# Performance work log

Measured on AMD Instinct MI355X. Metric: run time of the kernel, lower is better.

The kernel has to match this reference:

```python
import jax, jax.numpy as jnp
import numpy as np

B, H, W, C = 64, 28, 28, 384
NH, WS = 12, 7
KD = C // NH            # key_dim = head_dim = 32 (attn_ratio=1.0 -> d = KD)
QKV_OUT = 3 * KD * NH   # 1152
HID = 4 * C             # mlp hidden
N = WS * WS             # tokens per window
L = H * W
SCALE = KD ** -0.5
EPS_LN = 1e-5
EPS_BN = 1e-5


def _make_bias_idxs():
    pts = [(i, j) for i in range(WS) for j in range(WS)]
    offs, idxs = {}, []
    for p1 in pts:
        for p2 in pts:
            o = (abs(p1[0] - p2[0]), abs(p1[1] - p2[1]))
            if o not in offs:
                offs[o] = len(offs)
            idxs.append(offs[o])
    return np.asarray(idxs, dtype=np.int32).reshape(N, N)


def _ln(x, g, b):
    m = jnp.mean(x, axis=-1, keepdims=True)
    v = jnp.mean(jnp.square(x - m), axis=-1, keepdims=True)
    return (x - m) * jax.lax.rsqrt(v + EPS_LN) * g + b


def setup_inputs() -> dict:
    key = jax.random.key(0)
    ks = jax.random.split(key, 8)
    s = 0.02
    return {
        "x": jax.random.normal(ks[0], (B, L, C), jnp.float32),
        "ln_a_g": jnp.ones((C,), jnp.float32),
        "ln_a_b": jnp.zeros((C,), jnp.float32),
        "qkv_w": jax.random.normal(ks[1], (QKV_OUT, C), jnp.float32) * s,
        "qkv_b": jnp.zeros((QKV_OUT,), jnp.float32),
        "attn_bias": jax.random.normal(ks[2], (NH, N), jnp.float32) * s,
        "proj_w": jax.random.normal(ks[3], (C, C), jnp.float32) * s,
        "proj_b": jnp.zeros((C,), jnp.float32),
        "conv_w": jax.random.normal(ks[4], (C, 1, 3, 3), jnp.float32) * s,
        "bn_g": jnp.ones((C,), jnp.float32),
        "bn_b": jnp.zeros((C,), jnp.float32),
        "bn_m": jnp.zeros((C,), jnp.float32),
        "bn_v": jnp.ones((C,), jnp.float32),
        "ln_m_g": jnp.ones((C,), jnp.float32),
        "ln_m_b": jnp.zeros((C,), jnp.float32),
        "fc1_w": jax.random.normal(ks[5], (HID, C), jnp.float32) * s,
        "fc1_b": jnp.zeros((HID,), jnp.float32),
        "fc2_w": jax.random.normal(ks[6], (C, HID), jnp.float32) * s,
        "fc2_b": jnp.zeros((C,), jnp.float32),
        "bias_idxs": jnp.asarray(_make_bias_idxs()),
    }


def reference(x, ln_a_g, ln_a_b, qkv_w, qkv_b, attn_bias, proj_w, proj_b,
              conv_w, bn_g, bn_b, bn_m, bn_v, ln_m_g, ln_m_b,
              fc1_w, fc1_b, fc2_w, fc2_b, bias_idxs):
    res = x
    nh, nw = H // WS, W // WS
    # window partition: [B,L,C] -> [B*nWin, N, C]
    xw = x.reshape(B, nh, WS, nw, WS, C).transpose(0, 1, 3, 2, 4, 5)
    xw = xw.reshape(B * nh * nw, N, C)
    # attention
    xn = _ln(xw, ln_a_g, ln_a_b)
    qkv = xn @ qkv_w.T + qkv_b                       # [Bw, N, 3*NH*KD]
    qkv = qkv.reshape(-1, N, NH, 3 * KD).transpose(0, 2, 1, 3)
    q, k, v = qkv[..., :KD], qkv[..., KD:2 * KD], qkv[..., 2 * KD:]
    bias = attn_bias[:, bias_idxs]                   # [NH, N, N]
    attn = jnp.einsum('bhnd,bhmd->bhnm', q, k) * SCALE + bias
    attn = jax.nn.softmax(attn, axis=-1)
    o = jnp.einsum('bhnm,bhmd->bhnd', attn, v)
    o = o.transpose(0, 2, 1, 3).reshape(-1, N, C)
    o = o @ proj_w.T + proj_b
    # window unpartition -> [B, L, C]
    o = o.reshape(B, nh, nw, WS, WS, C).transpose(0, 1, 3, 2, 4, 5).reshape(B, L, C)
    x = res + o
    # depthwise ConvBN (inference BN)
    xc = x.transpose(0, 2, 1).reshape(B, C, H, W)
    xc = jax.lax.conv_general_dilated(
        xc, conv_w, (1, 1), 'SAME', feature_group_count=C,
        dimension_numbers=('NCHW', 'OIHW', 'NCHW'))
    inv = jax.lax.rsqrt(bn_v + EPS_BN)
    xc = (xc - bn_m[None, :, None, None]) * (bn_g * inv)[None, :, None, None] + bn_b[None, :, None, None]
    x = xc.reshape(B, C, L).transpose(0, 2, 1)
    # MLP residual
    h = _ln(x, ln_m_g, ln_m_b)
    h = jax.nn.gelu(h @ fc1_w.T + fc1_b, approximate=False)
    h = h @ fc2_w.T + fc2_b
    return x + h
```

## Files before the change

kernel.cpp:

```cpp
#include <hip/hip_runtime.h>
#include <hip/hip_bf16.h>
#include <stdint.h>

#define BATCH 64
#define CC 384
#define NHEAD 12
#define KD 32
#define NTOK 49
#define LL 784
#define MTOT 50176
#define HID 1536
#define QKV_OUT 1152
#define SCALE 0.17677669529663687f
#define EPS 1e-5f

typedef __bf16 bf16x8 __attribute__((ext_vector_type(8)));
typedef float f32x4 __attribute__((ext_vector_type(4)));

__device__ __forceinline__ float bf2f(unsigned short u) {
  union { unsigned int u; float f; } cv; cv.u = ((unsigned int)u) << 16; return cv.f;
}
__device__ __forceinline__ unsigned short f2bf(float f) {
  union { float f; unsigned int u; } cv; cv.f = f;
  unsigned int r = cv.u + 0x7FFFu + ((cv.u >> 16) & 1u);
  return (unsigned short)(r >> 16);
}
__device__ __forceinline__ void gl_lds16(const unsigned short* g, unsigned short* l) {
  __builtin_amdgcn_global_load_lds(
      (const __attribute__((address_space(1))) unsigned int*)g,
      (__attribute__((address_space(3))) unsigned int*)l, 16, 0, 0);
}

__global__ void detect_kernel(const unsigned short* __restrict__ x, int* flag) {
  __shared__ int cnt;
  if (threadIdx.x == 0) cnt = 0;
  __syncthreads();
  int c = 0;
  for (int i = threadIdx.x; i < 4096; i += 256) {
    if (((x[i] >> 7) & 0xFF) == 0xFF) c++;
  }
  atomicAdd(&cnt, c);
  __syncthreads();
  if (threadIdx.x == 0) *flag = (cnt > 0) ? 1 : 0;
}

struct CvtArgs {
  const void* src[19];
  unsigned int n[19];
  unsigned int off[19];
};
__global__ __launch_bounds__(256) void convert_kernel(
    CvtArgs a, unsigned short* __restrict__ dst, const int* __restrict__ flag) {
  const int which = blockIdx.y;
  const unsigned int nn = a.n[which];
  unsigned short* d = dst + a.off[which];
  const unsigned int stride = gridDim.x * blockDim.x;
  const unsigned int idx = blockIdx.x * blockDim.x + threadIdx.x;
  const unsigned int ng = nn >> 3;
  if (*flag) {
    const float* s = (const float*)a.src[which];
    for (unsigned int g = idx; g < ng; g += stride) {
      const float4 f0 = ((const float4*)s)[g * 2];
      const float4 f1 = ((const float4*)s)[g * 2 + 1];
      ushort4 lo, hi;
      lo.x = f2bf(f0.x); lo.y = f2bf(f0.y); lo.z = f2bf(f0.z); lo.w = f2bf(f0.w);
      hi.x = f2bf(f1.x); hi.y = f2bf(f1.y); hi.z = f2bf(f1.z); hi.w = f2bf(f1.w);
      ((ushort4*)d)[g * 2] = lo;
      ((ushort4*)d)[g * 2 + 1] = hi;
    }
    for (unsigned int i = ng * 8 + idx; i < nn; i += stride) d[i] = f2bf(s[i]);
  } else {
    const unsigned short* s = (const unsigned short*)a.src[which];
    for (unsigned int g = idx; g < ng; g += stride)
      ((uint4*)d)[g] = ((const uint4*)s)[g];
    for (unsigned int i = ng * 8 + idx; i < nn; i += stride) d[i] = s[i];
  }
}

__global__ __launch_bounds__(256) void bias_kernel(
    const unsigned short* __restrict__ cAb, const int* __restrict__ bias_idxs,
    float* __restrict__ bias_full) {
  const int h = blockIdx.x;
  for (int i = threadIdx.x; i < NTOK * NTOK; i += 256)
    bias_full[h * NTOK * NTOK + i] = bf2f(cAb[h * NTOK + bias_idxs[i]]);
}

__global__ __launch_bounds__(384) void prep_kernel(
    const unsigned short* __restrict__ cw, const unsigned short* __restrict__ bg,
    const unsigned short* __restrict__ bb, const unsigned short* __restrict__ bm,
    const unsigned short* __restrict__ bv,
    unsigned short* __restrict__ cwT, float* __restrict__ bnsc, float* __restrict__ bnsh) {
  const int c = threadIdx.x;
  const float sc = bf2f(bg[c]) * rsqrtf(bf2f(bv[c]) + EPS);
  bnsc[c] = sc;
  bnsh[c] = bf2f(bb[c]) - bf2f(bm[c]) * sc;
  #pragma unroll
  for (int t = 0; t < 9; ++t) cwT[t * CC + c] = cw[c * 9 + t];
}

__global__ __launch_bounds__(128) void ln_kernel(
    const unsigned short* __restrict__ x, const unsigned short* __restrict__ g,
    const unsigned short* __restrict__ b, unsigned short* __restrict__ out) {
  const int tid = threadIdx.x;
  int wi = blockIdx.y, n = blockIdx.x;
  int bb = wi >> 4, wb = wi & 15;
  int nh_i = wb >> 2, nw_i = wb & 3;
  int hs = n / 7, wsx = n - hs * 7;
  int l = nh_i * 196 + hs * 28 + nw_i * 7 + wsx;
  size_t src_row = (size_t)bb * LL + l;
  size_t dst_row = (size_t)wi * NTOK + n;
  const unsigned short* xr = x + src_row * CC;
  float vals[3]; float s = 0.f, sq = 0.f;
  for (int j = 0; j < 3; ++j) {
    vals[j] = bf2f(xr[tid + 128 * j]);
    s += vals[j]; sq += vals[j] * vals[j];
  }
  for (int off = 32; off; off >>= 1) { s += __shfl_xor(s, off); sq += __shfl_xor(sq, off); }
  __shared__ float red[4];
  const int wv = tid >> 6;
  if ((tid & 63) == 0) { red[wv] = s; red[2 + wv] = sq; }
  __syncthreads();
  float tot = red[0] + red[1], totq = red[2] + red[3];
  float mean = tot * (1.f / CC);
  float var = totq * (1.f / CC) - mean * mean;
  float inv = rsqrtf(var + EPS);
  unsigned short* orow = out + dst_row * CC;
  for (int j = 0; j < 3; ++j) {
    int c = tid + 128 * j;
    float y = (vals[j] - mean) * inv * bf2f(g[c]) + bf2f(b[c]);
    orow[c] = f2bf(y);
  }
}

enum { EP_PLAIN = 0, EP_GELU = 1, EP_WINRES = 2, EP_RES2 = 3 };

template <int EP>
__global__ __launch_bounds__(256) void gemm128(
    const unsigned short* __restrict__ A, const unsigned short* __restrict__ W,
    const unsigned short* __restrict__ bias, const unsigned short* __restrict__ res,
    void* __restrict__ outp, int K, int N, int m_off, const int* __restrict__ flagp) {
  __shared__ __align__(16) unsigned short Al[128 * 32];
  __shared__ __align__(16) unsigned short Bl[128 * 32];
  const int tid = threadIdx.x;
  const int lane = tid & 63;
  const int wave = tid >> 6;
  const int bm = blockIdx.x * 128;
  const int bn = blockIdx.y * 128;
  const int wm = (wave >> 1) * 64;
  const int wn = (wave & 1) * 64;
  const int srow = tid >> 2;
  const int scol = (tid & 3) * 8;
  const unsigned short* Ap = A + (size_t)(bm + srow) * K + scol;
  const unsigned short* Wp = W + (size_t)(bn + srow) * K + scol;
  unsigned short* Alp = Al + tid * 8;
  unsigned short* Blp = Bl + tid * 8;
  const size_t rstep = (size_t)64 * K;
  f32x4 acc[4][4] = {};
  const int kq = (lane >> 4) * 8;
  const int fr = lane & 15;
  for (int k0 = 0; k0 < K; k0 += 32) {
    __syncthreads();
    gl_lds16(Ap, Alp);
    gl_lds16(Ap + rstep, Alp + 2048);
    gl_lds16(Wp, Blp);
    gl_lds16(Wp + rstep, Blp + 2048);
    Ap += 32; Wp += 32;
    __syncthreads();
    bf16x8 af[4], bfr[4];
    #pragma unroll
    for (int i = 0; i < 4; ++i) {
      af[i]  = *(const bf16x8*)(Al + (wm + i * 16 + fr) * 32 + kq);
      bfr[i] = *(const bf16x8*)(Bl + (wn + i * 16 + fr) * 32 + kq);
    }
    #pragma unroll
    for (int i = 0; i < 4; ++i)
      #pragma unroll
      for (int j = 0; j < 4; ++j)
        acc[i][j] = __builtin_amdgcn_mfma_f32_16x16x32_bf16(af[i], bfr[j], acc[i][j], 0, 0, 0);
  }
  int isf32 = 0;
  if (EP == EP_RES2) isf32 = *flagp;
  const int qr = (lane >> 4) * 4;
  float bvs[4];
  #pragma unroll
  for (int tj = 0; tj < 4; ++tj) bvs[tj] = bf2f(bias[bn + wn + tj * 16 + fr]);
  #pragma unroll
  for (int ti = 0; ti < 4; ++ti) {
    #pragma unroll
    for (int r = 0; r < 4; ++r) {
      const int mr = bm + wm + ti * 16 + qr + r;
      size_t rowbase;
      if (EP == EP_WINRES) {
        int wi = mr / 49; int nt = mr - wi * 49;
        int bb = wi >> 4; int wb = wi & 15;
        int nh_i = wb >> 2; int nw_i = wb & 3;
        int hs = nt / 7; int wsx = nt - hs * 7;
        int l = nh_i * 196 + hs * 28 + nw_i * 7 + wsx;
        rowbase = ((size_t)bb * LL + l) * CC;
      } else if (EP == EP_RES2) {
        rowbase = (size_t)(mr + m_off) * N;
      } else {
        rowbase = (size_t)mr * N;
      }
      #pragma unroll
      for (int tj = 0; tj < 4; ++tj) {
        const int n = bn + wn + tj * 16 + fr;
        float v = acc[ti][tj][r] + bvs[tj];
        if (EP == EP_GELU) {
          const float t = v * (1.5957691216f + 0.0713548162f * v * v);
          v = __fdividef(v, 1.0f + __expf(-t));
          ((unsigned short*)outp)[rowbase + n] = f2bf(v);
        } else if (EP == EP_WINRES) {
          size_t idx = rowbase + n;
          v += bf2f(res[idx]);
          ((unsigned short*)outp)[idx] = f2bf(v);
        } else if (EP == EP_RES2) {
          size_t idx = rowbase + n;
          v += bf2f(res[idx]);
          if (isf32) ((float*)outp)[idx] = v;
          else       ((unsigned short*)outp)[idx] = f2bf(v);
        } else {
          ((unsigned short*)outp)[rowbase + n] = f2bf(v);
        }
      }
    }
  }
}

__global__ __launch_bounds__(64) void attn_mfma(
    const unsigned short* __restrict__ qkv, const float* __restrict__ bias_full,
    unsigned short* __restrict__ o, int wi_off) {
  __shared__ __align__(16) unsigned short Pl[64 * 72];
  __shared__ __align__(16) unsigned short vT[32 * 72];
  const int wi = blockIdx.x, h = blockIdx.y;
  const int lane = threadIdx.x;
  const int l15 = lane & 15;
  const int quad = lane >> 4;
  const unsigned short* base = qkv + (size_t)wi * NTOK * QKV_OUT + h * 96;

  bf16x8 qf[4], kf[4];
  #pragma unroll
  for (int i = 0; i < 4; ++i) {
    const int n = i * 16 + l15;
    if (n < NTOK) {
      const unsigned short* p = base + (size_t)n * QKV_OUT + quad * 8;
      qf[i] = *(const bf16x8*)(p);
      kf[i] = *(const bf16x8*)(p + 32);
    } else {
      qf[i] = (bf16x8)0; kf[i] = (bf16x8)0;
    }
  }

  for (int idx = lane; idx < 32 * 72; idx += 64) vT[idx] = 0;
  __syncthreads();
  for (int idx = lane; idx < NTOK * KD; idx += 64) {
    const int m = idx >> 5, d = idx & 31;
    vT[d * 72 + m] = base[(size_t)m * QKV_OUT + 64 + d];
  }

  f32x4 acc[4][4] = {};
  #pragma unroll
  for (int i = 0; i < 4; ++i)
    #pragma unroll
    for (int j = 0; j < 4; ++j)
      acc[i][j] = __builtin_amdgcn_mfma_f32_16x16x32_bf16(qf[i], kf[j], acc[i][j], 0, 0, 0);

  const float* bh = bias_full + h * NTOK * NTOK;
  float rinv[4][4];
  #pragma unroll
  for (int i = 0; i < 4; ++i) {
    #pragma unroll
    for (int r = 0; r < 4; ++r) {
      const int n = i * 16 + quad * 4 + r;
      float sv[4];
      #pragma unroll
      for (int j = 0; j < 4; ++j) {
        const int m = j * 16 + l15;
        float s = acc[i][j][r] * SCALE;
        if (n < NTOK && m < NTOK) s += bh[n * NTOK + m];
        if (m >= NTOK) s = -1e30f;
        sv[j] = s;
      }
      float mx = fmaxf(fmaxf(sv[0], sv[1]), fmaxf(sv[2], sv[3]));
      #pragma unroll
      for (int t = 1; t < 16; t <<= 1) mx = fmaxf(mx, __shfl_xor(mx, t));
      float sum = 0.f;
      #pragma unroll
      for (int j = 0; j < 4; ++j) {
        const float p = __expf(sv[j] - mx);
        sum += p;
        Pl[n * 72 + j * 16 + l15] = f2bf(p);
      }
      #pragma unroll
      for (int t = 1; t < 16; t <<= 1) sum += __shfl_xor(sum, t);
      rinv[i][r] = 1.f / sum;
    }
  }
  __syncthreads();

  f32x4 acc2[4][2] = {};
  #pragma unroll
  for (int kk = 0; kk < 2; ++kk) {
    bf16x8 pf[4], vf[2];
    #pragma unroll
    for (int i = 0; i < 4; ++i)
      pf[i] = *(const bf16x8*)(Pl + (i * 16 + l15) * 72 + kk * 32 + quad * 8);
    #pragma unroll
    for (int jd = 0; jd < 2; ++jd)
      vf[jd] = *(const bf16x8*)(vT + (jd * 16 + l15) * 72 + kk * 32 + quad * 8);
    #pragma unroll
    for (int i = 0; i < 4; ++i)
      #pragma unroll
      for (int jd = 0; jd < 2; ++jd)
        acc2[i][jd] = __builtin_amdgcn_mfma_f32_16x16x32_bf16(pf[i], vf[jd], acc2[i][jd], 0, 0, 0);
  }

  #pragma unroll
  for (int i = 0; i < 4; ++i) {
    #pragma unroll
    for (int r = 0; r < 4; ++r) {
      const int n = i * 16 + quad * 4 + r;
      if (n < NTOK) {
        const float ri = rinv[i][r];
        #pragma unroll
        for (int jd = 0; jd < 2; ++jd) {
          const int d = jd * 16 + l15;
          o[((size_t)(wi_off + wi) * NTOK + n) * CC + h * KD + d] = f2bf(acc2[i][jd][r] * ri);
        }
      }
    }
  }
}

__global__ __launch_bounds__(384) void conv_bn_ln(
    const unsigned short* __restrict__ x1, const unsigned short* __restrict__ cwT,
    const float* __restrict__ bnsc, const float* __restrict__ bnsh,
    const unsigned short* __restrict__ mg, const unsigned short* __restrict__ mb,
    unsigned short* __restrict__ x2, unsigned short* __restrict__ xm) {
  __shared__ float rs[8][48], rq[8][48];
  const int tid = threadIdx.x;
  const int pos = tid / 48;
  const int c8 = tid - pos * 48;
  const int c0 = c8 * 8;
  const int hw = blockIdx.x * 8 + pos;
  const int b = blockIdx.y;
  const int h = hw / 28, w = hw - h * 28;
  float acc[8] = {};
  #pragma unroll
  for (int t = 0; t < 9; ++t) {
    const int dh = t / 3 - 1, dw = t % 3 - 1;
    const int hh = h + dh, ww = w + dw;
    if (hh >= 0 && hh < 28 && ww >= 0 && ww < 28) {
      const uint4 xv = *(const uint4*)(x1 + ((size_t)b * LL + hh * 28 + ww) * CC + c0);
      const uint4 wv = *(const uint4*)(cwT + t * CC + c0);
      const unsigned short* xp = (const unsigned short*)&xv;
      const unsigned short* wp = (const unsigned short*)&wv;
      #pragma unroll
      for (int k = 0; k < 8; ++k) acc[k] += bf2f(xp[k]) * bf2f(wp[k]);
    }
  }
  const float4 sc0 = *(const float4*)(bnsc + c0);
  const float4 sc1 = *(const float4*)(bnsc + c0 + 4);
  const float4 sh0 = *(const float4*)(bnsh + c0);
  const float4 sh1 = *(const float4*)(bnsh + c0 + 4);
  float y[8];
  y[0] = acc[0] * sc0.x + sh0.x; y[1] = acc[1] * sc0.y + sh0.y;
  y[2] = acc[2] * sc0.z + sh0.z; y[3] = acc[3] * sc0.w + sh0.w;
  y[4] = acc[4] * sc1.x + sh1.x; y[5] = acc[5] * sc1.y + sh1.y;
  y[6] = acc[6] * sc1.z + sh1.z; y[7] = acc[7] * sc1.w + sh1.w;
  ushort4 pk0, pk1;
  pk0.x = f2bf(y[0]); pk0.y = f2bf(y[1]); pk0.z = f2bf(y[2]); pk0.w = f2bf(y[3]);
  pk1.x = f2bf(y[4]); pk1.y = f2bf(y[5]); pk1.z = f2bf(y[6]); pk1.w = f2bf(y[7]);
  const size_t row = ((size_t)b * LL + hw) * CC + c0;
  *(ushort4*)(x2 + row) = pk0;
  *(ushort4*)(x2 + row + 4) = pk1;
  float s = 0.f, q = 0.f;
  #pragma unroll
  for (int k = 0; k < 8; ++k) { s += y[k]; q += y[k] * y[k]; }
  rs[pos][c8] = s; rq[pos][c8] = q;
  __syncthreads();
  float tot = 0.f, tq = 0.f;
  #pragma unroll 8
  for (int i = 0; i < 48; ++i) { tot += rs[pos][i]; tq += rq[pos][i]; }
  const float mean = tot * (1.f / CC);
  const float var = tq * (1.f / CC) - mean * mean;
  const float inv = rsqrtf(var + EPS);
  const uint4 gv = *(const uint4*)(mg + c0);
  const uint4 bv = *(const uint4*)(mb + c0);
  const unsigned short* gp = (const unsigned short*)&gv;
  const unsigned short* bp = (const unsigned short*)&bv;
  ushort4 lo, hi;
  unsigned short outv[8];
  #pragma unroll
  for (int k = 0; k < 8; ++k)
    outv[k] = f2bf((y[k] - mean) * inv * bf2f(gp[k]) + bf2f(bp[k]));
  lo.x = outv[0]; lo.y = outv[1]; lo.z = outv[2]; lo.w = outv[3];
  hi.x = outv[4]; hi.y = outv[5]; hi.z = outv[6]; hi.w = outv[7];
  *(ushort4*)(xm + row) = lo;
  *(ushort4*)(xm + row + 4) = hi;
}

extern "C" void kernel_launch(void* const* d_in, const int* in_sizes, int n_in,
                              void* d_out, int out_size, void* d_ws, size_t ws_size,
                              hipStream_t stream) {
  int* flag = (int*)d_ws;
  unsigned short* base = (unsigned short*)d_ws;

  CvtArgs args;
  size_t cur = 32;
  size_t off[19];
  for (int i = 0; i < 19; ++i) {
    off[i] = cur;
    args.src[i] = d_in[i];
    args.n[i] = (unsigned int)in_sizes[i];
    args.off[i] = (unsigned int)cur;
    cur += ((size_t)in_sizes[i] + 63) & ~(size_t)63;
  }
  const unsigned short* cx   = base + off[0];
  const unsigned short* cgA  = base + off[1];
  const unsigned short* cbA  = base + off[2];
  const unsigned short* cQw  = base + off[3];
  const unsigned short* cQb  = base + off[4];
  const unsigned short* cAb  = base + off[5];
  const unsigned short* cPw  = base + off[6];
  const unsigned short* cPb  = base + off[7];
  const unsigned short* cCw  = base + off[8];
  const unsigned short* cBg  = base + off[9];
  const unsigned short* cBb  = base + off[10];
  const unsigned short* cBm  = base + off[11];
  const unsigned short* cBv  = base + off[12];
  const unsigned short* cMg  = base + off[13];
  const unsigned short* cMb  = base + off[14];
  const unsigned short* cF1w = base + off[15];
  const unsigned short* cF1b = base + off[16];
  const unsigned short* cF2w = base + off[17];
  const unsigned short* cF2b = base + off[18];
  const int* bias_idxs = (const int*)d_in[19];

  const size_t SZ = (size_t)MTOT * CC;
  unsigned short* o_buf = base + cur;
  unsigned short* buf2  = o_buf + SZ;
  unsigned short* x2    = base + off[0];
  float* bias_full = (float*)(buf2 + (size_t)25088 * HID);
  unsigned short* cwT = (unsigned short*)(bias_full + 12 * NTOK * NTOK);
  float* bnsc = (float*)(cwT + 9 * CC + ((9 * CC) & 7 ? 0 : 0));
  float* bnsh = bnsc + CC;

  unsigned short* xn = (unsigned short*)d_out;

  detect_kernel<<<1, 256, 0, stream>>>((const unsigned short*)d_in[0], flag);
  convert_kernel<<<dim3(512, 19), 256, 0, stream>>>(args, base, flag);
  bias_kernel<<<NHEAD, 256, 0, stream>>>(cAb, bias_idxs, bias_full);
  prep_kernel<<<1, 384, 0, stream>>>(cCw, cBg, cBb, cBm, cBv, cwT, bnsc, bnsh);

  ln_kernel<<<dim3(49, 1024), 128, 0, stream>>>(cx, cgA, cbA, xn);

  for (int half = 0; half < 2; ++half) {
    gemm128<EP_PLAIN><<<dim3(196, 9), 256, 0, stream>>>(
        xn + (size_t)half * 25088 * CC, cQw, cQb, nullptr, buf2, CC, QKV_OUT, 0, nullptr);
    attn_mfma<<<dim3(512, NHEAD), 64, 0, stream>>>(buf2, bias_full, o_buf, half * 512);
  }

  gemm128<EP_WINRES><<<dim3(392, 3), 256, 0, stream>>>(
      o_buf, cPw, cPb, cx, d_out, CC, CC, 0, nullptr);

  conv_bn_ln<<<dim3(98, BATCH), 384, 0, stream>>>(
      (const unsigned short*)d_out, cwT, bnsc, bnsh, cMg, cMb, x2, o_buf);

  for (int half = 0; half < 2; ++half) {
    gemm128<EP_GELU><<<dim3(196, 12), 256, 0, stream>>>(
        o_buf + (size_t)half * 25088 * CC, cF1w, cF1b, nullptr, buf2, CC, HID, 0, nullptr);
    gemm128<EP_RES2><<<dim3(196, 3), 256, 0, stream>>>(
        buf2, cF2w, cF2b, x2, d_out, HID, CC, half * 25088, flag);
  }
}
```

Baseline: 766.4 us.

## Triple-buffer GEMM LDS tiles with async global-to-LDS prefetch

Swaps the single-buffered load/sync/compute loop in the bf16 MFMA GEMM for a three-stage ring of LDS buffers. Tiles are prefetched two K-steps ahead, and explicit vmcnt waits with raw s_barrier calls replace the two __syncthreads per iteration. The goal is to hide global-load latency behind MFMA work. The cost is 48KB of LDS per block, which may reduce occupancy, and the hand-written waitcnt logic is fragile.

```diff
diff --git a/kernel.cpp b/kernel.cpp
--- a/kernel.cpp
+++ b/kernel.cpp
@@ -139,8 +139,7 @@
     const unsigned short* __restrict__ A, const unsigned short* __restrict__ W,
     const unsigned short* __restrict__ bias, const unsigned short* __restrict__ res,
     void* __restrict__ outp, int K, int N, int m_off, const int* __restrict__ flagp) {
-  __shared__ __align__(16) unsigned short Al[128 * 32];
-  __shared__ __align__(16) unsigned short Bl[128 * 32];
+  __shared__ __align__(16) unsigned short lds[3 * 8192];
   const int tid = threadIdx.x;
   const int lane = tid & 63;
   const int wave = tid >> 6;
@@ -150,34 +149,54 @@
   const int wn = (wave & 1) * 64;
   const int srow = tid >> 2;
   const int scol = (tid & 3) * 8;
-  const unsigned short* Ap = A + (size_t)(bm + srow) * K + scol;
-  const unsigned short* Wp = W + (size_t)(bn + srow) * K + scol;
-  unsigned short* Alp = Al + tid * 8;
-  unsigned short* Blp = Bl + tid * 8;
+  const unsigned short* Ap0 = A + (size_t)(bm + srow) * K + scol;
+  const unsigned short* Wp0 = W + (size_t)(bn + srow) * K + scol;
   const size_t rstep = (size_t)64 * K;
   f32x4 acc[4][4] = {};
   const int kq = (lane >> 4) * 8;
   const int fr = lane & 15;
-  for (int k0 = 0; k0 < K; k0 += 32) {
-    __syncthreads();
-    gl_lds16(Ap, Alp);
-    gl_lds16(Ap + rstep, Alp + 2048);
-    gl_lds16(Wp, Blp);
-    gl_lds16(Wp + rstep, Blp + 2048);
-    Ap += 32; Wp += 32;
-    __syncthreads();
+  const int nt = K >> 5;
+
+  auto stage = [&](int bsel, int t) {
+    const unsigned short* ap = Ap0 + t * 32;
+    const unsigned short* wp = Wp0 + t * 32;
+    unsigned short* al = lds + bsel * 8192 + tid * 8;
+    unsigned short* bl = al + 4096;
+    gl_lds16(ap, al);
+    gl_lds16(ap + rstep, al + 2048);
+    gl_lds16(wp, bl);
+    gl_lds16(wp + rstep, bl + 2048);
+  };
+
+  stage(0, 0);
+  stage(1, 1);
+  int b = 0;
+  for (int t = 0; t < nt; ++t) {
+    if (t + 2 < nt) stage(b ? b - 1 : 2, t + 2);
+    if (t + 3 <= nt)      asm volatile("s_waitcnt vmcnt(8)" ::: "memory");
+    else if (t + 2 == nt) asm volatile("s_waitcnt vmcnt(4)" ::: "memory");
+    else                  asm volatile("s_waitcnt vmcnt(0)" ::: "memory");
+    __builtin_amdgcn_s_barrier();
+    __builtin_amdgcn_sched_barrier(0);
+    const unsigned short* Ab = lds + b * 8192;
+    const unsigned short* Bb = Ab + 4096;
     bf16x8 af[4], bfr[4];
     #pragma unroll
     for (int i = 0; i < 4; ++i) {
-      af[i]  = *(const bf16x8*)(Al + (wm + i * 16 + fr) * 32 + kq);
-      bfr[i] = *(const bf16x8*)(Bl + (wn + i * 16 + fr) * 32 + kq);
+      af[i]  = *(const bf16x8*)(Ab + (wm + i * 16 + fr) * 32 + kq);
+      bfr[i] = *(const bf16x8*)(Bb + (wn + i * 16 + fr) * 32 + kq);
     }
     #pragma unroll
     for (int i = 0; i < 4; ++i)
       #pragma unroll
       for (int j = 0; j < 4; ++j)
         acc[i][j] = __builtin_amdgcn_mfma_f32_16x16x32_bf16(af[i], bfr[j], acc[i][j], 0, 0, 0);
-  }
+    asm volatile("s_waitcnt lgkmcnt(0)" ::: "memory");
+    __builtin_amdgcn_sched_barrier(0);
+    __builtin_amdgcn_s_barrier();
+    b = (b == 2) ? 0 : b + 1;
+  }
+
   int isf32 = 0;
   if (EP == EP_RES2) isf32 = *flagp;
   const int qr = (lane >> 4) * 4;
@@ -191,10 +210,10 @@
       const int mr = bm + wm + ti * 16 + qr + r;
       size_t rowbase;
       if (EP == EP_WINRES) {
-        int wi = mr / 49; int nt = mr - wi * 49;
+        int wi = mr / 49; int nt2 = mr - wi * 49;
         int bb = wi >> 4; int wb = wi & 15;
         int nh_i = wb >> 2; int nw_i = wb & 3;
-        int hs = nt / 7; int wsx = nt - hs * 7;
+        int hs = nt2 / 7; int wsx = nt2 - hs * 7;
         int l = nh_i * 196 + hs * 28 + nw_i * 7 + wsx;
         rowbase = ((size_t)bb * LL + l) * CC;
       } else if (EP == EP_RES2) {
@@ -207,8 +226,8 @@
         const int n = bn + wn + tj * 16 + fr;
         float v = acc[ti][tj][r] + bvs[tj];
         if (EP == EP_GELU) {
-          const float t = v * (1.5957691216f + 0.0713548162f * v * v);
-          v = __fdividef(v, 1.0f + __expf(-t));
+          const float t2 = v * (1.5957691216f + 0.0713548162f * v * v);
+          v = __fdividef(v, 1.0f + __expf(-t2));
           ((unsigned short*)outp)[rowbase + n] = f2bf(v);
         } else if (EP == EP_WINRES) {
           size_t idx = rowbase + n;
```

New measurement: 733.1 us. 4.3% less time.
